# Kernel optimization log

Hardware: AMD Instinct MI355X
Metric: run time of the kernel (lower is better)

The kernel has to match this reference:

```python
import jax, jax.numpy as jnp
import numpy as np

NUM_CELLS = 15        # num_beams (polar bins over (-pi/2, pi/2])
NEIGH = 2.0           # neighborhood_size -> default fallback radius
P, B = 2048, 10000    # pedestrians, boundary points
EMB, HDIM, MID, BOT = 64, 64, 512, 1024


def setup_inputs() -> dict:
    key = jax.random.key(0)
    ks = jax.random.split(key, 8)
    def n(k, shp, s=1.0):
        return jax.random.normal(k, shp, dtype=jnp.float32) * s
    return {
        "h_states": n(ks[0], (1, P, HDIM)),
        "end_pos": n(ks[1], (P, 2), 4.0),
        "rel_pos": n(ks[2], (P, 2)),
        "boundary_points": n(ks[3], (B, 2), 5.0),
        "W_sp": n(ks[4], (2, EMB), 0.5),
        "b_sp": jnp.zeros((EMB,), jnp.float32),
        "W1": n(ks[5], (EMB + HDIM, MID), 0.05),
        "b1": jnp.zeros((MID,), jnp.float32),
        "g1": jnp.ones((MID,), jnp.float32),
        "be1": jnp.zeros((MID,), jnp.float32),
        "W2": n(ks[6], (MID, BOT), 0.05),
        "b2": jnp.zeros((BOT,), jnp.float32),
        "g2": jnp.ones((BOT,), jnp.float32),
        "be2": jnp.zeros((BOT,), jnp.float32),
    }


def _bn(x, g, b, eps=1e-5):
    # torch BatchNorm1d in training mode: biased batch statistics
    m = x.mean(axis=0)
    v = x.var(axis=0)
    return g * (x - m) * jax.lax.rsqrt(v + eps) + b


def _polar_grid(end_pos, rel_pos, bpts, nb, radius):
    # Vectorized replacement of the pandas pd.cut + groupby(...).idxmin path.
    Pn, Bn = end_pos.shape[0], bpts.shape[0]
    th_ped = jnp.arctan2(rel_pos[:, 1], rel_pos[:, 0])      # (P,)
    c, s = jnp.cos(th_ped)[:, None], jnp.sin(th_ped)[:, None]
    d = bpts[None, :, :] - end_pos[:, None, :]              # (P,B,2)
    xb = d[..., 0] * c + d[..., 1] * s                      # rotate into ped frame
    yb = -d[..., 0] * s + d[..., 1] * c
    r = jnp.sqrt(xb * xb + yb * yb)                         # (P,B)
    th = jnp.arctan2(yb, xb)                                # (P,B)

    width = np.pi / nb
    binid = jnp.clip(jnp.floor((th + np.pi / 2) / width).astype(jnp.int32), 0, nb - 1)
    valid = (th > -np.pi / 2) & (th <= np.pi / 2)           # pd.cut: (a, b] intervals
    pid = jnp.arange(Pn, dtype=jnp.int32)[:, None]
    dump = Pn * nb                                          # segment for out-of-range points
    seg = jnp.where(valid, pid * nb + binid, dump)          # (P,B)

    # appended fallback rows: one per (ped, bin) at bin-center angle, radius=neighborhood_size
    centers = jnp.linspace(-np.pi / 2 + np.pi / nb / 2,
                           np.pi / 2 - np.pi / nb / 2, nb).astype(jnp.float32)
    r_all = jnp.concatenate([r.ravel(), jnp.full((Pn * nb,), radius, jnp.float32)])
    th_all = jnp.concatenate([th.ravel(), jnp.tile(centers, Pn)])
    seg_all = jnp.concatenate([seg.ravel(), jnp.arange(Pn * nb, dtype=jnp.int32)])

    ns = Pn * nb + 1
    rmin = jax.ops.segment_min(r_all, seg_all, num_segments=ns)
    # argmin with first-occurrence tie-break (matches pandas idxmin ordering)
    N = r_all.shape[0]
    idx = jnp.arange(N, dtype=jnp.int32)
    cand = jnp.where(r_all <= rmin[seg_all], idx, N)
    arg = jax.ops.segment_min(cand, seg_all, num_segments=ns)[:Pn * nb]

    th_ch = th_all[arg].reshape(Pn, nb)
    r_ch = rmin[:Pn * nb].reshape(Pn, nb)
    xc = r_ch * jnp.cos(th_ch)
    yc = r_ch * jnp.sin(th_ch)
    # rotate back to world frame and translate
    x = xc * c - yc * s + end_pos[:, 0:1]
    y = xc * s + yc * c + end_pos[:, 1:2]
    return jnp.stack([x, y], axis=-1)                       # (P, nb, 2)


def reference(h_states, end_pos, rel_pos, boundary_points,
              W_sp, b_sp, W1, b1, g1, be1, W2, b2, g2, be2):
    cart = _polar_grid(end_pos, rel_pos, boundary_points, NUM_CELLS, NEIGH)
    rel_grid = (cart - end_pos[:, None, :]).reshape(-1, 2)  # (P*nb, 2)
    emb = rel_grid @ W_sp + b_sp                            # spatial_embedding
    h = h_states.reshape(-1, HDIM)                          # (P, h_dim)
    hid = jnp.repeat(h, NUM_CELLS, axis=0)                  # R1,R1,...,R2,R2,...
    x = jnp.concatenate([emb, hid], axis=1)                 # (P*nb, 128)
    x = jax.nn.relu(_bn(x @ W1 + b1, g1, be1))
    x = jax.nn.relu(_bn(x @ W2 + b2, g2, be2))
    return x.reshape(P, NUM_CELLS, BOT).max(axis=1)         # (P, bottleneck_dim)
```

## Files before the change

### kernel.cpp

```cpp
#include <hip/hip_runtime.h>
#include <hip/hip_bf16.h>
#include <math.h>

#define P_N   2048
#define B_N   10000
#define NB    15
#define MROWS (P_N * NB)
#define SPLIT 5
#define BPB   (B_N / SPLIT)

typedef __bf16 bf16x8 __attribute__((ext_vector_type(8)));
typedef float  f32x4  __attribute__((ext_vector_type(4)));

__device__ __forceinline__ float bf2f(unsigned short u) {
    union { unsigned int i; float f; } v; v.i = ((unsigned int)u) << 16; return v.f;
}
__device__ __forceinline__ unsigned short f2bf(float f) {
    union { float f; unsigned int i; } v; v.f = f;
    unsigned int i = v.i;
    i += 0x7FFFu + ((i >> 16) & 1u);
    return (unsigned short)(i >> 16);
}
__device__ __forceinline__ void gld_lds16(const unsigned short* g, unsigned short* l) {
    __builtin_amdgcn_global_load_lds(
        (const __attribute__((address_space(1))) unsigned int*)g,
        (__attribute__((address_space(3))) unsigned int*)l, 16, 0, 0);
}
__device__ __forceinline__ unsigned fkey(float f) {
    unsigned b = __float_as_uint(f);
    return (b & 0x80000000u) ? ~b : (b | 0x80000000u);
}
__device__ __forceinline__ float funkey(unsigned key) {
    unsigned b = (key & 0x80000000u) ? (key ^ 0x80000000u) : ~key;
    return __uint_as_float(b);
}

__global__ __launch_bounds__(256) void k_front(const float* __restrict__ W1,
        const float* __restrict__ W2, unsigned short* __restrict__ w1t,
        unsigned short* __restrict__ w2t, float* __restrict__ stats,
        const float* __restrict__ end_pos, const float* __restrict__ rel_pos,
        const float* __restrict__ bpts, unsigned long long* __restrict__ pkeys,
        const float* __restrict__ h, unsigned short* __restrict__ hbf,
        const float* __restrict__ Wsp, const float* __restrict__ bsp,
        const float* __restrict__ b1, float* __restrict__ V0,
        float* __restrict__ V1, float* __restrict__ cvec) {
    __shared__ unsigned short t[64][65];
    __shared__ unsigned long long s_key[4][16];
    int blk = blockIdx.x, tid = threadIdx.x;
    if (blk < 144) {
        const float* W; unsigned short* O; int NC, K, tr, tc;
        if (blk < 16) { W = W1; O = w1t; NC = 512; K = 128; tr = blk & 1; tc = blk >> 1; }
        else { int b = blk - 16; W = W2; O = w2t; NC = 1024; K = 512; tr = b & 7; tc = b >> 3; }
        int r0 = tr * 64, c0 = tc * 64;
        int cx = tid & 63, rg = tid >> 6;
#pragma unroll
        for (int i = 0; i < 16; ++i) {
            int r = rg * 16 + i;
            t[r][cx] = f2bf(W[(size_t)(r0 + r) * NC + c0 + cx]);
        }
        __syncthreads();
#pragma unroll
        for (int i = 0; i < 16; ++i) {
            int n = rg * 16 + i;
            O[(size_t)(c0 + n) * K + r0 + cx] = t[cx][n];
        }
    } else if (blk < 2196) {
        int zidx = (blk - 144) * 256 + tid;
        if (zidx < 525056) {
            uint4 z = {0u, 0u, 0u, 0u};
            ((uint4*)stats)[zidx] = z;
        }
    } else if (blk < 2198) {
        int col = (blk - 2196) * 256 + tid;
        float v0 = 0.f, v1 = 0.f, cc = 0.f;
        for (int e = 0; e < 64; ++e) {
            float w = W1[(size_t)e * 512 + col];
            v0 = fmaf(Wsp[e], w, v0);
            v1 = fmaf(Wsp[64 + e], w, v1);
            cc = fmaf(bsp[e], w, cc);
        }
        V0[col] = v0; V1[col] = v1; cvec[col] = cc + b1[col];
    } else if (blk < 2326) {
        int base = (blk - 2198) * 1024 + tid * 4;
        float4 hv = *(const float4*)(h + base);
        unsigned short ub[4] = {f2bf(hv.x), f2bf(hv.y), f2bf(hv.z), f2bf(hv.w)};
        *(uint2*)(hbf + base) = *(uint2*)ub;
    } else {
        int sb = blk - 2326;
        int pg = sb / SPLIT, part = sb % SPLIT;
        int p0 = pg * 4;
        if (tid < 64) s_key[tid >> 4][tid & 15] = ~0ull;
        __syncthreads();

        float ex[4], ey[4], cr[4], sr[4];
#pragma unroll
        for (int pi = 0; pi < 4; ++pi) {
            ex[pi] = end_pos[2 * (p0 + pi)];
            ey[pi] = end_pos[2 * (p0 + pi) + 1];
            float rx = rel_pos[2 * (p0 + pi)], ry = rel_pos[2 * (p0 + pi) + 1];
            float rr = rx * rx + ry * ry;
            if (rr > 0.0f) { float inv = 1.0f / sqrtf(rr); cr[pi] = rx * inv; sr[pi] = ry * inv; }
            else           { cr[pi] = 1.0f; sr[pi] = 0.0f; }
        }

        const float T0 = -4.704630109f, T1 = -2.246036774f, T2 = -1.376381920f,
                    T3 = -0.900404044f, T4 = -0.577350269f, T5 = -0.324919696f,
                    T6 = -0.105104235f, T7 =  0.105104235f, T8 =  0.324919696f,
                    T9 =  0.577350269f, T10 = 0.900404044f, T11 = 1.376381920f,
                    T12 = 2.246036774f, T13 = 4.704630109f;

        const float2* bp2 = (const float2*)bpts;
        int bstart = part * BPB;
        for (int b = bstart + tid; b < bstart + BPB; b += 256) {
            float2 pt = bp2[b];
#pragma unroll
            for (int pi = 0; pi < 4; ++pi) {
                float dx = pt.x - ex[pi], dy = pt.y - ey[pi];
                float r2u = fmaf(dx, dx, dy * dy);
                if (r2u <= 4.0001f) {
                    float c = cr[pi], s = sr[pi];
                    float xb = dx * c + dy * s;
                    float yb = dy * c - dx * s;
                    if (xb > 0.0f) {
                        float r2 = fmaf(xb, xb, yb * yb);
                        bool v3 = yb > T7 * xb;
                        float ta = v3 ? T11 : T3;
                        bool v2 = yb > ta * xb;
                        float tb = v3 ? (v2 ? T13 : T9) : (v2 ? T5 : T1);
                        bool v1 = yb > tb * xb;
                        float tc = v3 ? (v2 ? (v1 ? 3.0e38f : T12) : (v1 ? T10 : T8))
                                      : (v2 ? (v1 ? T6 : T4)       : (v1 ? T2 : T0));
                        bool v0 = yb > tc * xb;
                        int bin = (v3 ? 8 : 0) + (v2 ? 4 : 0) + (v1 ? 2 : 0) + (v0 ? 1 : 0);
                        unsigned long long key =
                            ((unsigned long long)__float_as_uint(r2) << 32) | (unsigned int)b;
                        atomicMin(&s_key[pi][bin], key);
                    }
                }
            }
        }
        __syncthreads();
        if (tid < 64 && (tid & 15) < NB)
            pkeys[(size_t)part * MROWS + (p0 + (tid >> 4)) * NB + (tid & 15)] =
                s_key[tid >> 4][tid & 15];
    }
}

__global__ __launch_bounds__(64) void k_assemble(
        const unsigned long long* __restrict__ pkeys,
        const float* __restrict__ end_pos, const float* __restrict__ rel_pos,
        const float* __restrict__ bpts, float* __restrict__ rel,
        float* __restrict__ pm0, float* __restrict__ pm1, float* __restrict__ pm2,
        float* __restrict__ pm3, float* __restrict__ pm4) {
    int p = blockIdx.x, tid = threadIdx.x;
    float relx = 0.f, rely = 0.f;
    if (tid < NB) {
        float ex = end_pos[2 * p], ey = end_pos[2 * p + 1];
        unsigned long long key = ~0ull;
#pragma unroll
        for (int part = 0; part < SPLIT; ++part) {
            unsigned long long k = pkeys[(size_t)part * MROWS + p * NB + tid];
            key = (k < key) ? k : key;
        }
        float r = sqrtf(__uint_as_float((unsigned int)(key >> 32)));
        if (r <= 2.0f) {
            int b = (int)(key & 0xFFFFFFFFu);
            relx = bpts[2 * b] - ex; rely = bpts[2 * b + 1] - ey;
        } else {
            float rx = rel_pos[2 * p], ry = rel_pos[2 * p + 1];
            float rr = rx * rx + ry * ry;
            float c, s;
            if (rr > 0.0f) { float inv = 1.0f / sqrtf(rr); c = rx * inv; s = ry * inv; }
            else           { c = 1.0f; s = 0.0f; }
            float th = ((float)tid + 0.5f) * (float)(M_PI / 15.0) - (float)(M_PI / 2.0);
            float xc = 2.0f * cosf(th), yc = 2.0f * sinf(th);
            relx = xc * c - yc * s;
            rely = xc * s + yc * c;
        }
        rel[(size_t)(p * NB + tid) * 2]     = relx;
        rel[(size_t)(p * NB + tid) * 2 + 1] = rely;
    }
    float m0 = relx, m1 = rely, m2 = relx * relx, m3 = relx * rely, m4 = rely * rely;
#pragma unroll
    for (int d = 32; d >= 1; d >>= 1) {
        m0 += __shfl_xor(m0, d); m1 += __shfl_xor(m1, d);
        m2 += __shfl_xor(m2, d); m3 += __shfl_xor(m3, d);
        m4 += __shfl_xor(m4, d);
    }
    if (tid == 0) { pm0[p] = m0; pm1[p] = m1; pm2[p] = m2; pm3[p] = m3; pm4[p] = m4; }
}

__global__ __launch_bounds__(512) void k_hgemm(const unsigned short* __restrict__ hbf,
        const unsigned short* __restrict__ w1t, float* __restrict__ Hp,
        const float* __restrict__ V0, const float* __restrict__ V1,
        const float* __restrict__ cvec,
        const float* __restrict__ pm0, const float* __restrict__ pm1,
        const float* __restrict__ pm2, const float* __restrict__ pm3,
        const float* __restrict__ pm4,
        float* __restrict__ s1, float* __restrict__ q1) {
    __shared__ __align__(16) unsigned short lds[24576];
    int tid = threadIdx.x;
    int bm = blockIdx.x & 15, bnn = blockIdx.x >> 4;
    int row0 = bm << 7, col0 = bnn << 8;
    int lane = tid & 63, wave = tid >> 6;
    int wr = wave >> 2, wc = wave & 3;
    int frow = lane & 15, kq = lane >> 4;

    f32x4 zero = {0.f, 0.f, 0.f, 0.f};
    f32x4 acc[4][4];
#pragma unroll
    for (int i = 0; i < 4; ++i)
#pragma unroll
        for (int j = 0; j < 4; ++j) acc[i][j] = zero;

#pragma unroll
    for (int k = 0; k < 6; ++k) {
        int ch = wave * 6 + k;
        int s = (ch >= 24) ? 1 : 0;
        int r = ch - s * 24;
        unsigned short* dst = lds + s * 12288 + r * 512;
        const unsigned short* src =
            (r < 8) ? (hbf + (size_t)(row0 + r * 16 + frow) * 64 + s * 32 + kq * 8)
                    : (w1t + (size_t)(col0 + (r - 8) * 16 + frow) * 128 + 64 + s * 32 + kq * 8);
        gld_lds16(src, dst);
    }
    asm volatile("s_waitcnt vmcnt(0)" ::: "memory");
    __builtin_amdgcn_s_barrier();
    asm volatile("" ::: "memory");

#pragma unroll
    for (int s = 0; s < 2; ++s) {
        const unsigned short* sub = lds + s * 12288;
        bf16x8 af[4], bfv[4];
#pragma unroll
        for (int i = 0; i < 4; ++i)
            af[i] = *(const bf16x8*)&sub[(wr * 4 + i) * 512 + kq * 128 + frow * 8];
#pragma unroll
        for (int j = 0; j < 4; ++j)
            bfv[j] = *(const bf16x8*)&sub[4096 + (wc * 4 + j) * 512 + kq * 128 + frow * 8];
#pragma unroll
        for (int i = 0; i < 4; ++i)
#pragma unroll
            for (int j = 0; j < 4; ++j)
                acc[i][j] = __builtin_amdgcn_mfma_f32_16x16x32_bf16(af[i], bfv[j], acc[i][j], 0, 0, 0);
    }

    float v0c[4], v1c[4], cc[4];
#pragma unroll
    for (int j = 0; j < 4; ++j) {
        int col = col0 + wc * 64 + j * 16 + frow;
        v0c[j] = V0[col]; v1c[j] = V1[col]; cc[j] = cvec[col];
    }
    float csum[4] = {0.f, 0.f, 0.f, 0.f}, csq[4] = {0.f, 0.f, 0.f, 0.f};
#pragma unroll
    for (int i = 0; i < 4; ++i) {
#pragma unroll
        for (int r = 0; r < 4; ++r) {
            int row = row0 + wr * 64 + i * 16 + kq * 4 + r;
            float srx = pm0[row], sry = pm1[row];
            float sxx = pm2[row], sxy = pm3[row], syy = pm4[row];
#pragma unroll
            for (int j = 0; j < 4; ++j) {
                int col = col0 + wc * 64 + j * 16 + frow;
                float hp = acc[i][j][r];
                Hp[(size_t)row * 512 + col] = hp;
                float A  = hp + cc[j];
                float B1 = fmaf(srx, v0c[j], sry * v1c[j]);
                float B2 = fmaf(v0c[j] * v0c[j], sxx,
                           fmaf(2.0f * v0c[j] * v1c[j], sxy, v1c[j] * v1c[j] * syy));
                csum[j] += fmaf(15.0f, A, B1);
                csq[j]  += fmaf(15.0f, A * A, fmaf(2.0f * A, B1, B2));
            }
        }
    }
#pragma unroll
    for (int j = 0; j < 4; ++j) {
        int col = col0 + wc * 64 + j * 16 + frow;
        float cs = csum[j], cq = csq[j];
        cs += __shfl_xor(cs, 16); cs += __shfl_xor(cs, 32);
        cq += __shfl_xor(cq, 16); cq += __shfl_xor(cq, 32);
        if (lane < 16) { atomicAdd(&s1[col], cs); atomicAdd(&q1[col], cq); }
    }
}

__global__ __launch_bounds__(256) void k_y1w(const float* __restrict__ Hp,
        const float* __restrict__ rel, const float* __restrict__ V0,
        const float* __restrict__ V1, const float* __restrict__ cvec,
        const float* __restrict__ s1, const float* __restrict__ q1,
        const float* __restrict__ g1, const float* __restrict__ be1,
        unsigned short* __restrict__ Y1) {
    int tid = threadIdx.x;
    int p = blockIdx.x;
    int seg = tid & 63, cg = tid >> 6;
    const float invN = 1.0f / (float)MROWS;
    float4 ha = *(const float4*)(Hp + (size_t)p * 512 + seg * 8);
    float4 hb = *(const float4*)(Hp + (size_t)p * 512 + seg * 8 + 4);
    float4 ca = *(const float4*)(cvec + seg * 8);
    float4 cb = *(const float4*)(cvec + seg * 8 + 4);
    float4 va = *(const float4*)(V0 + seg * 8), vb = *(const float4*)(V0 + seg * 8 + 4);
    float4 wa = *(const float4*)(V1 + seg * 8), wb = *(const float4*)(V1 + seg * 8 + 4);
    float hc[8] = {ha.x+ca.x, ha.y+ca.y, ha.z+ca.z, ha.w+ca.w,
                   hb.x+cb.x, hb.y+cb.y, hb.z+cb.z, hb.w+cb.w};
    float v0[8] = {va.x,va.y,va.z,va.w,vb.x,vb.y,vb.z,vb.w};
    float v1[8] = {wa.x,wa.y,wa.z,wa.w,wb.x,wb.y,wb.z,wb.w};
    float sc[8], sh[8];
#pragma unroll
    for (int j = 0; j < 8; ++j) {
        int ccix = seg * 8 + j;
        float m = s1[ccix] * invN;
        float v = q1[ccix] * invN - m * m;
        float k = g1[ccix] * rsqrtf(v + 1e-5f);
        sc[j] = k; sh[j] = be1[ccix] - m * k;
    }
#pragma unroll
    for (int i = 0; i < 4; ++i) {
        int cell = cg + i * 4;
        if (cell < NB) {
            float2 rl = *(const float2*)(rel + (size_t)(p * NB + cell) * 2);
            unsigned short ub[8];
#pragma unroll
            for (int j = 0; j < 8; ++j) {
                float y = fmaf(rl.x, v0[j], fmaf(rl.y, v1[j], hc[j]));
                float z = fmaxf(fmaf(y, sc[j], sh[j]), 0.0f);
                ub[j] = f2bf(z);
            }
            *(uint4*)(Y1 + (size_t)(p * NB + cell) * 512 + seg * 8) = *(uint4*)ub;
        }
    }
}

template<int K, bool WRITE_C>
__global__ __launch_bounds__(512) void k_gemm256(
        const unsigned short* __restrict__ A, const unsigned short* __restrict__ Bt,
        const float* __restrict__ bias, unsigned short* __restrict__ C,
        int N, float* __restrict__ osum, float* __restrict__ osq,
        unsigned int* __restrict__ mkey) {
    __shared__ __align__(16) unsigned short lds[65536];
    int tid = threadIdx.x;

    int nbt = N >> 8;
    int d = blockIdx.x;
    int m5 = d >> 3;
    int bn = m5 % nbt;
    int bm = (d & 7) + ((m5 / nbt) << 3);
    int row0 = bm << 8, col0 = bn << 8;

    int lane = tid & 63, wave = tid >> 6;
    int wr = wave >> 2, wc = wave & 3;
    int frow = lane & 15, kq = lane >> 4;

    f32x4 zero = {0.f, 0.f, 0.f, 0.f};
    f32x4 acc[8][4];
#pragma unroll
    for (int i = 0; i < 8; ++i)
#pragma unroll
        for (int j = 0; j < 4; ++j) acc[i][j] = zero;

    const unsigned short* gsrc =
        (wave < 4) ? (A  + (size_t)(row0 + (wave << 6) + frow) * K + kq * 8)
                   : (Bt + (size_t)(col0 + ((wave - 4) << 6) + frow) * K + kq * 8);
    unsigned regbase = (wave < 4) ? (unsigned)wave * 2048
                                  : 8192u + (unsigned)(wave - 4) * 2048;

    auto issue2 = [&](int t, int s, int hp) {
        unsigned short* dst = lds + (t & 1) * 32768 + s * 16384 + regbase + hp * 1024;
        const unsigned short* src = gsrc + t * 64 + s * 32 + (size_t)(hp * 32) * K;
        gld_lds16(src,                  dst);
        gld_lds16(src + (size_t)16 * K, dst + 512);
    };

    constexpr int NT = K / 64;
    static_assert(NT >= 2, "need >=2 K-tiles");

    issue2(0, 0, 0); issue2(0, 0, 1); issue2(0, 1, 0); issue2(0, 1, 1);

#pragma unroll
    for (int t = 0; t < NT; ++t) {
        const unsigned short* buf = lds + (t & 1) * 32768;
        bool more = (t + 1 < NT);
#pragma unroll
        for (int s = 0; s < 2; ++s) {
            const unsigned short* sub = buf + s * 16384;
            if (more || s == 0) asm volatile("s_waitcnt vmcnt(4)" ::: "memory");
            else                asm volatile("s_waitcnt vmcnt(0)" ::: "memory");
            __builtin_amdgcn_s_barrier();
            asm volatile("" ::: "memory");
            bf16x8 bfv[4], af[4];
#pragma unroll
            for (int j = 0; j < 4; ++j)
                bfv[j] = *(const bf16x8*)&sub[8192 + (wc * 4 + j) * 512 + kq * 128 + frow * 8];
#pragma unroll
            for (int i = 0; i < 4; ++i)
                af[i] = *(const bf16x8*)&sub[(wr * 8 + i) * 512 + kq * 128 + frow * 8];
            if (more) issue2(t + 1, s, 0);
            __builtin_amdgcn_s_barrier();
            asm volatile("" ::: "memory");
            __builtin_amdgcn_s_setprio(1);
#pragma unroll
            for (int i = 0; i < 4; ++i)
#pragma unroll
                for (int j = 0; j < 4; ++j)
                    acc[i][j] = __builtin_amdgcn_mfma_f32_16x16x32_bf16(af[i], bfv[j], acc[i][j], 0, 0, 0);
            __builtin_amdgcn_s_setprio(0);
#pragma unroll
            for (int i = 0; i < 4; ++i)
                af[i] = *(const bf16x8*)&sub[(wr * 8 + 4 + i) * 512 + kq * 128 + frow * 8];
            if (more) issue2(t + 1, s, 1);
            __builtin_amdgcn_s_barrier();
            asm volatile("" ::: "memory");
            __builtin_amdgcn_s_setprio(1);
#pragma unroll
            for (int i = 0; i < 4; ++i)
#pragma unroll
                for (int j = 0; j < 4; ++j)
                    acc[4 + i][j] = __builtin_amdgcn_mfma_f32_16x16x32_bf16(af[i], bfv[j], acc[4 + i][j], 0, 0, 0);
            __builtin_amdgcn_s_setprio(0);
        }
    }

    float bv[4];
#pragma unroll
    for (int j = 0; j < 4; ++j) bv[j] = bias[col0 + wc * 64 + j * 16 + frow];

#pragma unroll
    for (int j = 0; j < 4; ++j) {
        int col = col0 + wc * 64 + j * 16 + frow;
        float csum = 0.f, csq = 0.f;
#pragma unroll
        for (int i = 0; i < 8; ++i) {
#pragma unroll
            for (int r = 0; r < 4; ++r) {
                float y = acc[i][j][r] + bv[j];
                csum += y; csq = fmaf(y, y, csq);
            }
        }
        csum += __shfl_xor(csum, 16); csum += __shfl_xor(csum, 32);
        csq  += __shfl_xor(csq, 16);  csq  += __shfl_xor(csq, 32);
        if (lane < 16) { atomicAdd(&osum[col], csum); atomicAdd(&osq[col], csq); }
    }

    unsigned short* ldsC = lds;
#pragma unroll
    for (int b = 0; b < 4; ++b) {
        __syncthreads();
        if (wr == (b >> 1)) {
#pragma unroll
            for (int j = 0; j < 4; ++j) {
#pragma unroll
                for (int ii = 0; ii < 4; ++ii) {
                    int i = (b & 1) * 4 + ii;
#pragma unroll
                    for (int r = 0; r < 4; ++r) {
                        float y = acc[i][j][r] + bv[j];
                        ldsC[(ii * 16 + kq * 4 + r) * 264 + wc * 64 + j * 16 + frow] = f2bf(y);
                    }
                }
            }
        }
        __syncthreads();
        if (WRITE_C) {
#pragma unroll
            for (int it = 0; it < 4; ++it) {
                int s = it * 512 + tid;
                int brow = s >> 5, seg = s & 31;
                *(uint4*)(C + (size_t)(row0 + b * 64 + brow) * N + col0 + seg * 8) =
                    *(const uint4*)&ldsC[brow * 264 + seg * 8];
            }
        } else {
            int col = tid & 255, half = tid >> 8;
            int lrow0 = half * 32;
            int grow = row0 + b * 64 + lrow0;
            int curp = grow / 15;
            int rem = 15 - (grow - curp * 15);
            float mx = -3.0e38f;
#pragma unroll
            for (int r = 0; r < 32; ++r) {
                mx = fmaxf(mx, bf2f(ldsC[(lrow0 + r) * 264 + col]));
                if (--rem == 0) {
                    atomicMax(&mkey[(size_t)curp * 1024 + col0 + col], fkey(mx));
                    mx = -3.0e38f; ++curp; rem = 15;
                }
            }
            if (rem != 15)
                atomicMax(&mkey[(size_t)curp * 1024 + col0 + col], fkey(mx));
        }
    }
}

__global__ void k_bnfin(const unsigned int* __restrict__ mkey, const float* __restrict__ s2,
                        const float* __restrict__ q2, const float* __restrict__ g2,
                        const float* __restrict__ be2, float* __restrict__ out) {
    int idx = blockIdx.x * 256 + threadIdx.x;
    int p = idx >> 7, cb = idx & 127;
    int c0 = cb << 3;
    const float invN = 1.0f / (float)MROWS;
    float4 sa = *(const float4*)(s2 + c0),  sb = *(const float4*)(s2 + c0 + 4);
    float4 qa = *(const float4*)(q2 + c0),  qb = *(const float4*)(q2 + c0 + 4);
    float4 ga = *(const float4*)(g2 + c0),  gb = *(const float4*)(g2 + c0 + 4);
    float4 ea = *(const float4*)(be2 + c0), eb = *(const float4*)(be2 + c0 + 4);
    float sv[8] = {sa.x,sa.y,sa.z,sa.w,sb.x,sb.y,sb.z,sb.w};
    float qv[8] = {qa.x,qa.y,qa.z,qa.w,qb.x,qb.y,qb.z,qb.w};
    float gv[8] = {ga.x,ga.y,ga.z,ga.w,gb.x,gb.y,gb.z,gb.w};
    float ev[8] = {ea.x,ea.y,ea.z,ea.w,eb.x,eb.y,eb.z,eb.w};
    uint4 k0 = *(const uint4*)(mkey + (size_t)p * 1024 + c0);
    uint4 k1 = *(const uint4*)(mkey + (size_t)p * 1024 + c0 + 4);
    unsigned kv[8] = {k0.x,k0.y,k0.z,k0.w,k1.x,k1.y,k1.z,k1.w};
    float o[8];
#pragma unroll
    for (int j = 0; j < 8; ++j) {
        float m = sv[j] * invN;
        float v = qv[j] * invN - m * m;
        float k = gv[j] * rsqrtf(v + 1e-5f);
        float sh = ev[j] - m * k;
        o[j] = fmaxf(fmaf(funkey(kv[j]), k, sh), 0.0f);
    }
    float4 o0 = {o[0], o[1], o[2], o[3]};
    float4 o1 = {o[4], o[5], o[6], o[7]};
    *(float4*)(out + (size_t)p * 1024 + c0)     = o0;
    *(float4*)(out + (size_t)p * 1024 + c0 + 4) = o1;
}

extern "C" void kernel_launch(void* const* d_in, const int* in_sizes, int n_in,
                              void* d_out, int out_size, void* d_ws, size_t ws_size,
                              hipStream_t stream) {
    const float* h       = (const float*)d_in[0];
    const float* end_pos = (const float*)d_in[1];
    const float* rel_pos = (const float*)d_in[2];
    const float* bpts    = (const float*)d_in[3];
    const float* Wsp     = (const float*)d_in[4];
    const float* bsp     = (const float*)d_in[5];
    const float* W1      = (const float*)d_in[6];
    const float* b1      = (const float*)d_in[7];
    const float* g1      = (const float*)d_in[8];
    const float* be1     = (const float*)d_in[9];
    const float* W2      = (const float*)d_in[10];
    const float* b2      = (const float*)d_in[11];
    const float* g2      = (const float*)d_in[12];
    const float* be2     = (const float*)d_in[13];
    float* out = (float*)d_out;

    char* ws = (char*)d_ws;
    float* s1  = (float*)ws;
    float* q1  = s1 + 512;
    float* s2  = q1 + 512;
    float* q2  = s2 + 1024;
    unsigned int* mkey        = (unsigned int*)(ws + 12288);
    unsigned long long* pkeys = (unsigned long long*)(ws + 12288 + 8388608);
    unsigned short* w1t = (unsigned short*)(ws + 9629696);
    unsigned short* w2t = (unsigned short*)(ws + 9760768);
    unsigned short* hbf = (unsigned short*)(ws + 10809344);
    float* V0   = (float*)(ws + 11071488);
    float* V1   = V0 + 512;
    float* cvec = V1 + 512;
    float* Hp   = (float*)(ws + 11081728);
    float* rel  = (float*)(ws + 15276032);
    unsigned short* Y1 = (unsigned short*)(ws + 15521792);
    float* pm0 = (float*)(ws + 46979072);
    float* pm1 = pm0 + 2048;
    float* pm2 = pm1 + 2048;
    float* pm3 = pm2 + 2048;
    float* pm4 = pm3 + 2048;

    k_front<<<4886, 256, 0, stream>>>(W1, W2, w1t, w2t, s1, end_pos, rel_pos,
                                      bpts, pkeys, h, hbf, Wsp, bsp, b1, V0, V1, cvec);
    k_assemble<<<P_N, 64, 0, stream>>>(pkeys, end_pos, rel_pos, bpts, rel,
                                       pm0, pm1, pm2, pm3, pm4);
    k_hgemm<<<32, 512, 0, stream>>>(hbf, w1t, Hp, V0, V1, cvec,
                                    pm0, pm1, pm2, pm3, pm4, s1, q1);
    k_y1w<<<P_N, 256, 0, stream>>>(Hp, rel, V0, V1, cvec, s1, q1, g1, be1, Y1);
    k_gemm256<512, false><<<(MROWS / 256) * (1024 / 256), 512, 0, stream>>>(
        Y1, w2t, b2, nullptr, 1024, s2, q2, mkey);
    k_bnfin<<<(P_N * 128) / 256, 256, 0, stream>>>(mkey, s2, q2, g2, be2, out);
}
```

Before: 111.8 us.

## Shrink second GEMM tile to 128x256 with smaller LDS for higher occupancy

Replaces the 256x256 GEMM tile with a 128x256 tile that uses K-steps of 32 and a simpler double-buffered LDS pipeline (48KB down to 24K shorts). Halving the accumulators and LDS footprint, plus launch_bounds(512,4), is meant to allow more resident blocks per CU and to double the grid size, improving latency hiding and load balance. In exchange there are more barriers per K and lower arithmetic intensity per tile, and the epilogue writes to LDS and the max reduction now span 128-row tiles.

Measured after the change: 120.5 us. 1.08x slower.

```diff
diff --git a/kernel.cpp b/kernel.cpp
--- a/kernel.cpp
+++ b/kernel.cpp
@@ -330,12 +330,12 @@
 }
 
 template<int K, bool WRITE_C>
-__global__ __launch_bounds__(512) void k_gemm256(
+__global__ __launch_bounds__(512, 4) void k_gemm2(
         const unsigned short* __restrict__ A, const unsigned short* __restrict__ Bt,
         const float* __restrict__ bias, unsigned short* __restrict__ C,
         int N, float* __restrict__ osum, float* __restrict__ osq,
         unsigned int* __restrict__ mkey) {
-    __shared__ __align__(16) unsigned short lds[65536];
+    __shared__ __align__(16) unsigned short lds[24576];
     int tid = threadIdx.x;
 
     int nbt = N >> 8;
@@ -343,79 +343,58 @@
     int m5 = d >> 3;
     int bn = m5 % nbt;
     int bm = (d & 7) + ((m5 / nbt) << 3);
-    int row0 = bm << 8, col0 = bn << 8;
+    int row0 = bm << 7, col0 = bn << 8;
 
     int lane = tid & 63, wave = tid >> 6;
     int wr = wave >> 2, wc = wave & 3;
     int frow = lane & 15, kq = lane >> 4;
 
     f32x4 zero = {0.f, 0.f, 0.f, 0.f};
-    f32x4 acc[8][4];
-#pragma unroll
-    for (int i = 0; i < 8; ++i)
+    f32x4 acc[4][4];
+#pragma unroll
+    for (int i = 0; i < 4; ++i)
 #pragma unroll
         for (int j = 0; j < 4; ++j) acc[i][j] = zero;
 
-    const unsigned short* gsrc =
-        (wave < 4) ? (A  + (size_t)(row0 + (wave << 6) + frow) * K + kq * 8)
-                   : (Bt + (size_t)(col0 + ((wave - 4) << 6) + frow) * K + kq * 8);
-    unsigned regbase = (wave < 4) ? (unsigned)wave * 2048
-                                  : 8192u + (unsigned)(wave - 4) * 2048;
-
-    auto issue2 = [&](int t, int s, int hp) {
-        unsigned short* dst = lds + (t & 1) * 32768 + s * 16384 + regbase + hp * 1024;
-        const unsigned short* src = gsrc + t * 64 + s * 32 + (size_t)(hp * 32) * K;
-        gld_lds16(src,                  dst);
-        gld_lds16(src + (size_t)16 * K, dst + 512);
+    auto issue = [&](int t) {
+        unsigned short* dstb = lds + (t & 1) * 12288;
+#pragma unroll
+        for (int k = 0; k < 3; ++k) {
+            int ch = wave * 3 + k;
+            const unsigned short* src = (ch < 8)
+                ? (A  + (size_t)(row0 + ch * 16 + frow) * K + t * 32 + kq * 8)
+                : (Bt + (size_t)(col0 + (ch - 8) * 16 + frow) * K + t * 32 + kq * 8);
+            gld_lds16(src, dstb + ch * 512);
+        }
     };
 
-    constexpr int NT = K / 64;
-    static_assert(NT >= 2, "need >=2 K-tiles");
-
-    issue2(0, 0, 0); issue2(0, 0, 1); issue2(0, 1, 0); issue2(0, 1, 1);
+    constexpr int NT = K / 32;
+    issue(0);
+    asm volatile("s_waitcnt vmcnt(0)" ::: "memory");
+    __builtin_amdgcn_s_barrier();
+    asm volatile("" ::: "memory");
 
 #pragma unroll
     for (int t = 0; t < NT; ++t) {
-        const unsigned short* buf = lds + (t & 1) * 32768;
-        bool more = (t + 1 < NT);
-#pragma unroll
-        for (int s = 0; s < 2; ++s) {
-            const unsigned short* sub = buf + s * 16384;
-            if (more || s == 0) asm volatile("s_waitcnt vmcnt(4)" ::: "memory");
-            else                asm volatile("s_waitcnt vmcnt(0)" ::: "memory");
-            __builtin_amdgcn_s_barrier();
-            asm volatile("" ::: "memory");
-            bf16x8 bfv[4], af[4];
+        if (t + 1 < NT) issue(t + 1);
+        const unsigned short* buf = lds + (t & 1) * 12288;
+        bf16x8 af[4], bfv[4];
+#pragma unroll
+        for (int i = 0; i < 4; ++i)
+            af[i] = *(const bf16x8*)&buf[(wr * 4 + i) * 512 + kq * 128 + frow * 8];
+#pragma unroll
+        for (int j = 0; j < 4; ++j)
+            bfv[j] = *(const bf16x8*)&buf[4096 + (wc * 4 + j) * 512 + kq * 128 + frow * 8];
+        __builtin_amdgcn_s_setprio(1);
+#pragma unroll
+        for (int i = 0; i < 4; ++i)
 #pragma unroll
             for (int j = 0; j < 4; ++j)
-                bfv[j] = *(const bf16x8*)&sub[8192 + (wc * 4 + j) * 512 + kq * 128 + frow * 8];
-#pragma unroll
-            for (int i = 0; i < 4; ++i)
-                af[i] = *(const bf16x8*)&sub[(wr * 8 + i) * 512 + kq * 128 + frow * 8];
-            if (more) issue2(t + 1, s, 0);
-            __builtin_amdgcn_s_barrier();
-            asm volatile("" ::: "memory");
-            __builtin_amdgcn_s_setprio(1);
-#pragma unroll
-            for (int i = 0; i < 4; ++i)
-#pragma unroll
-                for (int j = 0; j < 4; ++j)
-                    acc[i][j] = __builtin_amdgcn_mfma_f32_16x16x32_bf16(af[i], bfv[j], acc[i][j], 0, 0, 0);
-            __builtin_amdgcn_s_setprio(0);
-#pragma unroll
-            for (int i = 0; i < 4; ++i)
-                af[i] = *(const bf16x8*)&sub[(wr * 8 + 4 + i) * 512 + kq * 128 + frow * 8];
-            if (more) issue2(t + 1, s, 1);
-            __builtin_amdgcn_s_barrier();
-            asm volatile("" ::: "memory");
-            __builtin_amdgcn_s_setprio(1);
-#pragma unroll
-            for (int i = 0; i < 4; ++i)
-#pragma unroll
-                for (int j = 0; j < 4; ++j)
-                    acc[4 + i][j] = __builtin_amdgcn_mfma_f32_16x16x32_bf16(af[i], bfv[j], acc[4 + i][j], 0, 0, 0);
-            __builtin_amdgcn_s_setprio(0);
-        }
+                acc[i][j] = __builtin_amdgcn_mfma_f32_16x16x32_bf16(af[i], bfv[j], acc[i][j], 0, 0, 0);
+        __builtin_amdgcn_s_setprio(0);
+        asm volatile("s_waitcnt vmcnt(0)" ::: "memory");
+        __builtin_amdgcn_s_barrier();
+        asm volatile("" ::: "memory");
     }
 
     float bv[4];
@@ -427,7 +406,7 @@
         int col = col0 + wc * 64 + j * 16 + frow;
         float csum = 0.f, csq = 0.f;
 #pragma unroll
-        for (int i = 0; i < 8; ++i) {
+        for (int i = 0; i < 4; ++i) {
 #pragma unroll
             for (int r = 0; r < 4; ++r) {
                 float y = acc[i][j][r] + bv[j];
@@ -441,18 +420,17 @@
 
     unsigned short* ldsC = lds;
 #pragma unroll
-    for (int b = 0; b < 4; ++b) {
+    for (int b = 0; b < 2; ++b) {
         __syncthreads();
-        if (wr == (b >> 1)) {
+        if (wr == b) {
 #pragma unroll
             for (int j = 0; j < 4; ++j) {
 #pragma unroll
-                for (int ii = 0; ii < 4; ++ii) {
-                    int i = (b & 1) * 4 + ii;
+                for (int i = 0; i < 4; ++i) {
 #pragma unroll
                     for (int r = 0; r < 4; ++r) {
                         float y = acc[i][j][r] + bv[j];
-                        ldsC[(ii * 16 + kq * 4 + r) * 264 + wc * 64 + j * 16 + frow] = f2bf(y);
+                        ldsC[(i * 16 + kq * 4 + r) * 264 + wc * 64 + j * 16 + frow] = f2bf(y);
                     }
                 }
             }
@@ -568,7 +546,7 @@
     k_hgemm<<<32, 512, 0, stream>>>(hbf, w1t, Hp, V0, V1, cvec,
                                     pm0, pm1, pm2, pm3, pm4, s1, q1);
     k_y1w<<<P_N, 256, 0, stream>>>(Hp, rel, V0, V1, cvec, s1, q1, g1, be1, Y1);
-    k_gemm256<512, false><<<(MROWS / 256) * (1024 / 256), 512, 0, stream>>>(
+    k_gemm2<512, false><<<(MROWS / 128) * (1024 / 256), 512, 0, stream>>>(
         Y1, w2t, b2, nullptr, 1024, s2, q2, mkey);
     k_bnfin<<<(P_N * 128) / 256, 256, 0, stream>>>(mkey, s2, q2, g2, be2, out);
 }
```

## Fuse polar-grid assembly into front kernel and drop boundary split

Applied to the files above, without the earlier changes.

Removes the SPLIT=5 partition of boundary points so each polar-grid block scans all 10000 points for its 4 pedestrians, then finalizes the nearest-point selection, relative positions and per-pedestrian moment sums in the same block. This eliminates the k_assemble launch and the partial-key buffer round trip through global memory. The trade-off is fewer, longer-running blocks in the scan phase (512 instead of 2560), which reduces parallelism and may lengthen the front kernel's tail.

After: 128.6 us. 1.15x slower.

```diff
diff --git a/kernel.cpp b/kernel.cpp
--- a/kernel.cpp
+++ b/kernel.cpp
@@ -6,8 +6,6 @@
 #define B_N   10000
 #define NB    15
 #define MROWS (P_N * NB)
-#define SPLIT 5
-#define BPB   (B_N / SPLIT)
 
 typedef __bf16 bf16x8 __attribute__((ext_vector_type(8)));
 typedef float  f32x4  __attribute__((ext_vector_type(4)));
@@ -39,11 +37,14 @@
         const float* __restrict__ W2, unsigned short* __restrict__ w1t,
         unsigned short* __restrict__ w2t, float* __restrict__ stats,
         const float* __restrict__ end_pos, const float* __restrict__ rel_pos,
-        const float* __restrict__ bpts, unsigned long long* __restrict__ pkeys,
+        const float* __restrict__ bpts,
         const float* __restrict__ h, unsigned short* __restrict__ hbf,
         const float* __restrict__ Wsp, const float* __restrict__ bsp,
         const float* __restrict__ b1, float* __restrict__ V0,
-        float* __restrict__ V1, float* __restrict__ cvec) {
+        float* __restrict__ V1, float* __restrict__ cvec,
+        float* __restrict__ rel,
+        float* __restrict__ pm0, float* __restrict__ pm1, float* __restrict__ pm2,
+        float* __restrict__ pm3, float* __restrict__ pm4) {
     __shared__ unsigned short t[64][65];
     __shared__ unsigned long long s_key[4][16];
     int blk = blockIdx.x, tid = threadIdx.x;
@@ -86,8 +87,7 @@
         unsigned short ub[4] = {f2bf(hv.x), f2bf(hv.y), f2bf(hv.z), f2bf(hv.w)};
         *(uint2*)(hbf + base) = *(uint2*)ub;
     } else {
-        int sb = blk - 2326;
-        int pg = sb / SPLIT, part = sb % SPLIT;
+        int pg = blk - 2326;
         int p0 = pg * 4;
         if (tid < 64) s_key[tid >> 4][tid & 15] = ~0ull;
         __syncthreads();
@@ -110,8 +110,7 @@
                     T12 = 2.246036774f, T13 = 4.704630109f;
 
         const float2* bp2 = (const float2*)bpts;
-        int bstart = part * BPB;
-        for (int b = bstart + tid; b < bstart + BPB; b += 256) {
+        for (int b = tid; b < B_N; b += 256) {
             float2 pt = bp2[b];
 #pragma unroll
             for (int pi = 0; pi < 4; ++pi) {
@@ -140,54 +139,33 @@
             }
         }
         __syncthreads();
-        if (tid < 64 && (tid & 15) < NB)
-            pkeys[(size_t)part * MROWS + (p0 + (tid >> 4)) * NB + (tid & 15)] =
-                s_key[tid >> 4][tid & 15];
-    }
-}
-
-__global__ __launch_bounds__(64) void k_assemble(
-        const unsigned long long* __restrict__ pkeys,
-        const float* __restrict__ end_pos, const float* __restrict__ rel_pos,
-        const float* __restrict__ bpts, float* __restrict__ rel,
-        float* __restrict__ pm0, float* __restrict__ pm1, float* __restrict__ pm2,
-        float* __restrict__ pm3, float* __restrict__ pm4) {
-    int p = blockIdx.x, tid = threadIdx.x;
-    float relx = 0.f, rely = 0.f;
-    if (tid < NB) {
-        float ex = end_pos[2 * p], ey = end_pos[2 * p + 1];
-        unsigned long long key = ~0ull;
-#pragma unroll
-        for (int part = 0; part < SPLIT; ++part) {
-            unsigned long long k = pkeys[(size_t)part * MROWS + p * NB + tid];
-            key = (k < key) ? k : key;
-        }
-        float r = sqrtf(__uint_as_float((unsigned int)(key >> 32)));
-        if (r <= 2.0f) {
-            int b = (int)(key & 0xFFFFFFFFu);
-            relx = bpts[2 * b] - ex; rely = bpts[2 * b + 1] - ey;
-        } else {
-            float rx = rel_pos[2 * p], ry = rel_pos[2 * p + 1];
-            float rr = rx * rx + ry * ry;
-            float c, s;
-            if (rr > 0.0f) { float inv = 1.0f / sqrtf(rr); c = rx * inv; s = ry * inv; }
-            else           { c = 1.0f; s = 0.0f; }
-            float th = ((float)tid + 0.5f) * (float)(M_PI / 15.0) - (float)(M_PI / 2.0);
-            float xc = 2.0f * cosf(th), yc = 2.0f * sinf(th);
-            relx = xc * c - yc * s;
-            rely = xc * s + yc * c;
-        }
-        rel[(size_t)(p * NB + tid) * 2]     = relx;
-        rel[(size_t)(p * NB + tid) * 2 + 1] = rely;
-    }
-    float m0 = relx, m1 = rely, m2 = relx * relx, m3 = relx * rely, m4 = rely * rely;
-#pragma unroll
-    for (int d = 32; d >= 1; d >>= 1) {
-        m0 += __shfl_xor(m0, d); m1 += __shfl_xor(m1, d);
-        m2 += __shfl_xor(m2, d); m3 += __shfl_xor(m3, d);
-        m4 += __shfl_xor(m4, d);
-    }
-    if (tid == 0) { pm0[p] = m0; pm1[p] = m1; pm2[p] = m2; pm3[p] = m3; pm4[p] = m4; }
+        int wv = tid >> 6, lane = tid & 63;
+        int p = p0 + wv;
+        float relx = 0.f, rely = 0.f;
+        if (lane < NB) {
+            unsigned long long key = s_key[wv][lane];
+            float r = sqrtf(__uint_as_float((unsigned int)(key >> 32)));
+            if (r <= 2.0f) {
+                int b = (int)(key & 0xFFFFFFFFu);
+                relx = bpts[2 * b] - ex[wv]; rely = bpts[2 * b + 1] - ey[wv];
+            } else {
+                float th = ((float)lane + 0.5f) * (float)(M_PI / 15.0) - (float)(M_PI / 2.0);
+                float xc = 2.0f * cosf(th), yc = 2.0f * sinf(th);
+                relx = xc * cr[wv] - yc * sr[wv];
+                rely = xc * sr[wv] + yc * cr[wv];
+            }
+            rel[(size_t)(p * NB + lane) * 2]     = relx;
+            rel[(size_t)(p * NB + lane) * 2 + 1] = rely;
+        }
+        float m0 = relx, m1 = rely, m2 = relx * relx, m3 = relx * rely, m4 = rely * rely;
+#pragma unroll
+        for (int d = 32; d >= 1; d >>= 1) {
+            m0 += __shfl_xor(m0, d); m1 += __shfl_xor(m1, d);
+            m2 += __shfl_xor(m2, d); m3 += __shfl_xor(m3, d);
+            m4 += __shfl_xor(m4, d);
+        }
+        if (lane == 0) { pm0[p] = m0; pm1[p] = m1; pm2[p] = m2; pm3[p] = m3; pm4[p] = m4; }
+    }
 }
 
 __global__ __launch_bounds__(512) void k_hgemm(const unsigned short* __restrict__ hbf,
@@ -544,27 +522,25 @@
     float* q1  = s1 + 512;
     float* s2  = q1 + 512;
     float* q2  = s2 + 1024;
-    unsigned int* mkey        = (unsigned int*)(ws + 12288);
-    unsigned long long* pkeys = (unsigned long long*)(ws + 12288 + 8388608);
-    unsigned short* w1t = (unsigned short*)(ws + 9629696);
-    unsigned short* w2t = (unsigned short*)(ws + 9760768);
-    unsigned short* hbf = (unsigned short*)(ws + 10809344);
-    float* V0   = (float*)(ws + 11071488);
+    unsigned int* mkey  = (unsigned int*)(ws + 12288);
+    unsigned short* w1t = (unsigned short*)(ws + 8400896);
+    unsigned short* w2t = (unsigned short*)(ws + 8531968);
+    unsigned short* hbf = (unsigned short*)(ws + 9580544);
+    float* V0   = (float*)(ws + 9842688);
     float* V1   = V0 + 512;
     float* cvec = V1 + 512;
-    float* Hp   = (float*)(ws + 11081728);
-    float* rel  = (float*)(ws + 15276032);
-    unsigned short* Y1 = (unsigned short*)(ws + 15521792);
-    float* pm0 = (float*)(ws + 46979072);
+    float* Hp   = (float*)(ws + 9852928);
+    float* rel  = (float*)(ws + 14047232);
+    unsigned short* Y1 = (unsigned short*)(ws + 14292992);
+    float* pm0 = (float*)(ws + 45750272);
     float* pm1 = pm0 + 2048;
     float* pm2 = pm1 + 2048;
     float* pm3 = pm2 + 2048;
     float* pm4 = pm3 + 2048;
 
-    k_front<<<4886, 256, 0, stream>>>(W1, W2, w1t, w2t, s1, end_pos, rel_pos,
-                                      bpts, pkeys, h, hbf, Wsp, bsp, b1, V0, V1, cvec);
-    k_assemble<<<P_N, 64, 0, stream>>>(pkeys, end_pos, rel_pos, bpts, rel,
-                                       pm0, pm1, pm2, pm3, pm4);
+    k_front<<<2838, 256, 0, stream>>>(W1, W2, w1t, w2t, s1, end_pos, rel_pos,
+                                      bpts, h, hbf, Wsp, bsp, b1, V0, V1, cvec,
+                                      rel, pm0, pm1, pm2, pm3, pm4);
     k_hgemm<<<32, 512, 0, stream>>>(hbf, w1t, Hp, V0, V1, cvec,
                                     pm0, pm1, pm2, pm3, pm4, s1, q1);
     k_y1w<<<P_N, 256, 0, stream>>>(Hp, rel, V0, V1, cvec, s1, q1, g1, be1, Y1);
```
